# Kernel optimization log

Hardware: AMD Instinct MI355X
Metric: run time of the kernel (lower is better)

The kernel has to match this reference:

```python
import jax, jax.numpy as jnp
import numpy as np

BST_DEPTH = 10                      # tree depth
NB_SPLIT = 2 ** BST_DEPTH - 1       # 1023 internal (split) nodes
NB_NODES = 2 ** (BST_DEPTH + 1) - 1 # 2047 total nodes
N = 32768                           # batch size
IN_SIZE = 255                       # raw feature dim (dim = IN_SIZE + 1 after bias concat)


def setup_inputs() -> dict:
    key = jax.random.key(0)
    k1, k2, k3 = jax.random.split(key, 3)
    dim = IN_SIZE + 1
    X = jax.random.normal(k1, (N, IN_SIZE), dtype=jnp.float32)
    # A ~ U[0,1) as in torch.rand
    A = jax.random.uniform(k2, (NB_SPLIT, dim), dtype=jnp.float32)
    W = jax.random.normal(k3, (1, dim + NB_NODES), dtype=jnp.float32) * 0.02
    b = jnp.zeros((1,), dtype=jnp.float32)
    return {"X": X, "A": A, "W": W, "b": b}


def _latent_tree_z(x, A):
    """Equivalent of LatentTree._compute_q + clamp, unpruned.

    The torch code initializes q=1, scatters min(1, +/-XA) into children, then
    propagates parent mins down for `depth` iterations. The fixed point it
    reaches is exactly q_t = min(q_parent(t), sign_t * XA[:, parent(t)]) computed
    level by level (root q = 1), which is what we build here.
    """
    XA = x @ A.T  # [N, nb_split]
    n = x.shape[0]
    q_levels = [jnp.ones((n, 1), x.dtype)]  # root
    for l in range(1, BST_DEPTH + 1):
        t = np.arange(2 ** l - 1, 2 ** (l + 1) - 1)      # node ids at level l
        parent = (t - 1) // 2                            # split-node ids
        sign = np.where(t % 2 == 1, 1.0, -1.0).astype(np.float32)  # left:+, right:-
        e = XA[:, parent] * sign[None, :]                # edge values [N, 2^l]
        prev_off = 2 ** (l - 1) - 1
        q_parent = q_levels[-1][:, parent - prev_off]    # gather parent q
        q_levels.append(jnp.minimum(q_parent, e))
    q = jnp.concatenate(q_levels, axis=1)  # [N, nb_nodes]
    return jnp.clip(q, 0.0, 1.0)


def reference(X, A, W, b):
    # append bias column of ones
    x = jnp.concatenate([X, jnp.ones((X.shape[0], 1), X.dtype)], axis=1)
    z = _latent_tree_z(x, A)                 # [N, nb_nodes]
    xz = jnp.concatenate([x, z], axis=1)     # [N, dim + nb_nodes]
    return jax.nn.sigmoid(xz @ W.T + b)      # [N, 1]
```

## Files before the change

### kernel.cpp

```cpp
#include <hip/hip_runtime.h>

typedef __attribute__((ext_vector_type(8))) short    bf16x8;
typedef __attribute__((ext_vector_type(4))) float    f32x4;
typedef __attribute__((ext_vector_type(4))) float    float4_t;
typedef __attribute__((ext_vector_type(4))) unsigned u32x4;
typedef __attribute__((ext_vector_type(2))) unsigned u32x2;

constexpr int NSAMP    = 32768;
constexpr int INSZ     = 255;
constexpr int DIM      = 256;
constexpr int NSPLIT   = 1023;
constexpr int NCOL     = 1024;
constexpr int BM       = 32;
constexpr int NTHREADS = 256;
constexpr int NMT      = BM / 16;
constexpr int NPASS    = 64 / 4;

constexpr int XA_OFF    = 16384;
constexpr int PART_OFF  = 8192;
constexpr int PSTRIDE   = 64;
constexpr int LDS_BYTES = XA_OFF + BM * 2048;
constexpr size_t WS_NEED = (size_t)NCOL * DIM * 2;

extern __shared__ char smem[];

__device__ __forceinline__ short f2bf(float f) {
  unsigned x = __builtin_bit_cast(unsigned, f);
  x += 0x7fffu + ((x >> 16) & 1u);
  return (short)(x >> 16);
}
__device__ __forceinline__ float bfraw(unsigned hw16) {
  return __builtin_bit_cast(float, hw16 << 16);
}
__device__ __forceinline__ unsigned cvt_pk(float lo, float hi) {
  unsigned r;
  asm("v_cvt_pk_bf16_f32 %0, %1, %2" : "=v"(r) : "v"(lo), "v"(hi));
  return r;
}
__device__ __forceinline__ float clamp01(float v) {
  return fminf(fmaxf(v, 0.f), 1.f);
}

__global__ void prep_frag(const float* __restrict__ A, const float* __restrict__ W,
                          u32x4* __restrict__ wsf)
{
  int t    = blockIdx.x * 512 + threadIdx.x;
  int lane = t & 63;
  int ks   = (t >> 6) & 7;
  int ct   = t >> 9;
  int col  = ct * 16 + (lane & 15);
  int k0   = ks * 32 + ((lane >> 4) << 3);
  const float* src = (col < NSPLIT) ? (A + col * DIM + k0) : (W + k0);
  float4_t a0 = *(const float4_t*)src;
  float4_t a1 = *(const float4_t*)(src + 4);
  u32x4 p;
  p[0] = cvt_pk(a0[0], a0[1]);
  p[1] = cvt_pk(a0[2], a0[3]);
  p[2] = cvt_pk(a1[0], a1[1]);
  p[3] = cvt_pk(a1[2], a1[3]);
  wsf[t] = p;
}

template<bool USE_WS>
__device__ __forceinline__ void load_bfr(int ct, bf16x8* dst, int lane,
                                         const u32x4* __restrict__ wsf,
                                         const float* __restrict__ A,
                                         const float* __restrict__ W)
{
  if constexpr (USE_WS) {
    const u32x4* fp = wsf + ct * 512 + lane;
#pragma unroll
    for (int ks = 0; ks < 8; ++ks)
      dst[ks] = __builtin_bit_cast(bf16x8, fp[ks * 64]);
  } else {
    int col = ct * 16 + (lane & 15);
    int k0  = (lane >> 4) << 3;
    const float* ap = (col < NSPLIT) ? (A + col * DIM) : W;
#pragma unroll
    for (int ks = 0; ks < 8; ++ks) {
      float4_t a0 = *(const float4_t*)(ap + ks * 32 + k0);
      float4_t a1 = *(const float4_t*)(ap + ks * 32 + k0 + 4);
      u32x4 p;
      p[0] = cvt_pk(a0[0], a0[1]);
      p[1] = cvt_pk(a0[2], a0[3]);
      p[2] = cvt_pk(a1[0], a1[1]);
      p[3] = cvt_pk(a1[2], a1[3]);
      dst[ks] = __builtin_bit_cast(bf16x8, p);
    }
  }
}

__device__ __forceinline__ float walk(const char* __restrict__ xar, int swz, int lane,
                                      const float* __restrict__ wl,
                                      float w7a, float w7b,
                                      const float* __restrict__ w8r,
                                      const float* __restrict__ w9r,
                                      const float* __restrict__ wAr)
{
  float acc = 0.f;
  float q   = 1.0f;
#pragma unroll
  for (int l = 1; l <= 6; ++l) {
    float qp = __shfl(q, lane >> 1, 64);
    int  pos = (1 << (l - 1)) + (lane >> 1);
    unsigned hw = *(const unsigned short*)(xar + (((pos << 1)) ^ swz));
    float xa = bfraw(hw);
    float e  = (lane & 1) ? -xa : xa;
    q = fminf(qp, e);
    acc += clamp01(q) * wl[l - 1];
  }
  unsigned h7 = *(const unsigned short*)(xar + ((((64 + lane) << 1)) ^ swz));
  float xa7 = bfraw(h7);
  float q7a = fminf(q, xa7), q7b = fminf(q, -xa7);
  acc += clamp01(q7a) * w7a + clamp01(q7b) * w7b;
  unsigned u8 = *(const unsigned*)(xar + (((256 + 4 * lane)) ^ swz));
  float x8a = bfraw(u8 & 0xffffu), x8b = bfraw(u8 >> 16);
  float q8[4];
  q8[0] = fminf(q7a, x8a);  q8[1] = fminf(q7a, -x8a);
  q8[2] = fminf(q7b, x8b);  q8[3] = fminf(q7b, -x8b);
#pragma unroll
  for (int c = 0; c < 4; ++c) acc += clamp01(q8[c]) * w8r[c];
  u32x2 u9 = *(const u32x2*)(xar + (((512 + 8 * lane)) ^ swz));
  float x9[4] = { bfraw(u9[0] & 0xffffu), bfraw(u9[0] >> 16),
                  bfraw(u9[1] & 0xffffu), bfraw(u9[1] >> 16) };
  float q9[8];
#pragma unroll
  for (int c = 0; c < 8; ++c)
    q9[c] = fminf(q8[c >> 1], (c & 1) ? -x9[c >> 1] : x9[c >> 1]);
#pragma unroll
  for (int c = 0; c < 8; ++c) acc += clamp01(q9[c]) * w9r[c];
  u32x4 uAB = *(const u32x4*)(xar + (((1024 + 16 * lane)) ^ swz));
  float xA[8] = { bfraw(uAB[0] & 0xffffu), bfraw(uAB[0] >> 16),
                  bfraw(uAB[1] & 0xffffu), bfraw(uAB[1] >> 16),
                  bfraw(uAB[2] & 0xffffu), bfraw(uAB[2] >> 16),
                  bfraw(uAB[3] & 0xffffu), bfraw(uAB[3] >> 16) };
#pragma unroll
  for (int c = 0; c < 16; ++c) {
    float qv = fminf(q9[c >> 1], (c & 1) ? -xA[c >> 1] : xA[c >> 1]);
    acc += clamp01(qv) * wAr[c];
  }
  return acc;
}

template<bool USE_WS>
__global__ __launch_bounds__(NTHREADS) __attribute__((amdgpu_waves_per_eu(2, 2)))
void lt_main(const float* __restrict__ X, const float* __restrict__ A,
             const float* __restrict__ W, const float* __restrict__ Bv,
             const u32x4* __restrict__ wsf, float* __restrict__ Out)
{
  const int tid  = threadIdx.x;
  const int lane = tid & 63;
  const int wave = tid >> 6;
  const int m0   = blockIdx.x * BM;

  bf16x8 b0[8], b1[8];
  load_bfr<USE_WS>(wave, b0, lane, wsf, A, W);

  float wl[6], w8r[4], w9r[8], wAr[16];
#pragma unroll
  for (int l = 1; l <= 6; ++l)
    wl[l - 1] = (lane < (1 << l)) ? W[DIM + (1 << l) - 1 + lane] : 0.f;
  float w7a = W[DIM + 127 + 2 * lane];
  float w7b = W[DIM + 128 + 2 * lane];
#pragma unroll
  for (int e = 0; e < 4; ++e)  w8r[e] = W[DIM + 255 + 4 * lane + e];
#pragma unroll
  for (int e = 0; e < 8; ++e)  w9r[e] = W[DIM + 511 + 8 * lane + e];
#pragma unroll
  for (int e = 0; e < 16; ++e) wAr[e] = W[DIM + 1023 + 16 * lane + e];

  {
    const float4_t* Xt = (const float4_t*)(X + (size_t)m0 * INSZ);
#pragma unroll
    for (int i = 0; i < 8; ++i) {
      int idx = tid + i * NTHREADS;
      if (idx < 2040) {
        float4_t v = Xt[idx];
#pragma unroll
        for (int e = 0; e < 4; ++e) {
          int g   = idx * 4 + e;
          int row = g / 255;
          int col = g - row * 255;
          *(short*)(smem + (((row << 9) + (col << 1)) ^ ((row & 7) << 4))) = f2bf(v[e]);
        }
      }
    }
    if (tid < BM)
      *(short*)(smem + (((tid << 9) + (255 << 1)) ^ ((tid & 7) << 4))) = (short)0x3f80;
  }
  __syncthreads();

  bf16x8 xf[NMT][8];
#pragma unroll
  for (int mt = 0; mt < NMT; ++mt) {
    int row = mt * 16 + (lane & 15);
#pragma unroll
    for (int ks = 0; ks < 8; ++ks) {
      int kk = ks * 32 + ((lane >> 4) << 3);
      xf[mt][ks] = *(const bf16x8*)(smem + (((row << 9) + (kk << 1)) ^ ((row & 7) << 4)));
    }
  }

#pragma unroll
  for (int p = 0; p < NPASS; ++p) {
    bf16x8* cur = (p & 1) ? b1 : b0;
    bf16x8* nxt = (p & 1) ? b0 : b1;
    if (p < NPASS - 1)
      load_bfr<USE_WS>((p + 1) * 4 + wave, nxt, lane, wsf, A, W);

    f32x4 acc[NMT];
#pragma unroll
    for (int mt = 0; mt < NMT; ++mt) acc[mt] = f32x4{0.f, 0.f, 0.f, 0.f};
#pragma unroll
    for (int ks = 0; ks < 8; ++ks) {
#pragma unroll
      for (int mt = 0; mt < NMT; ++mt)
        acc[mt] = __builtin_amdgcn_mfma_f32_16x16x32_bf16(xf[mt][ks], cur[ks], acc[mt], 0, 0, 0);
    }

    int col = (p * 4 + wave) * 16 + (lane & 15);
    int pos = (col < NSPLIT) ? (col + 1) : 0;
#pragma unroll
    for (int mt = 0; mt < NMT; ++mt) {
#pragma unroll
      for (int j = 0; j < 4; ++j) {
        int row = mt * 16 + ((lane >> 4) << 2) + j;
        int byt = XA_OFF + (row << 11) + (((pos << 1)) ^ (((row >> 2) & 3) << 5));
        *(short*)(smem + byt) = f2bf(acc[mt][j]);
      }
    }
  }
  __syncthreads();

  float* part = (float*)(smem + PART_OFF);

#pragma unroll
  for (int t = 0; t < 4; ++t) {
    int rA = wave * 8 + 2 * t;
    int rB = rA + 1;
    const char* xarA = smem + XA_OFF + (rA << 11);
    const char* xarB = smem + XA_OFF + (rB << 11);
    const int swzA = ((rA >> 2) & 3) << 5;
    const int swzB = ((rB >> 2) & 3) << 5;
    float accA = walk(xarA, swzA, lane, wl, w7a, w7b, w8r, w9r, wAr);
    float accB = walk(xarB, swzB, lane, wl, w7a, w7b, w8r, w9r, wAr);
    part[rA * PSTRIDE + lane] = accA;
    part[rB * PSTRIDE + lane] = accB;
  }
  __syncthreads();

  {
    int r = tid >> 3, j = tid & 7;
    const float* pr = part + r * PSTRIDE + j * 8;
    float4_t s0 = *(const float4_t*)pr;
    float4_t s1 = *(const float4_t*)(pr + 4);
    float sum = ((s0[0] + s0[1]) + (s0[2] + s0[3]))
              + ((s1[0] + s1[1]) + (s1[2] + s1[3]));
    sum += __shfl_xor(sum, 1, 64);
    sum += __shfl_xor(sum, 2, 64);
    sum += __shfl_xor(sum, 4, 64);
    if (j == 0) {
      const char* xar = smem + XA_OFF + (r << 11);
      int swz = ((r >> 2) & 3) << 5;
      float xw = bfraw(*(const unsigned short*)(xar + (0 ^ swz)));
      float bias = Bv[0] + W[DIM];
      Out[m0 + r] = 1.f / (1.f + __expf(-(sum + xw + bias)));
    }
  }
}

extern "C" void kernel_launch(void* const* d_in, const int* in_sizes, int n_in,
                              void* d_out, int out_size, void* d_ws, size_t ws_size,
                              hipStream_t stream) {
  (void)in_sizes; (void)n_in; (void)out_size;
  const float* X  = (const float*)d_in[0];
  const float* A  = (const float*)d_in[1];
  const float* W  = (const float*)d_in[2];
  const float* Bv = (const float*)d_in[3];
  float* Out = (float*)d_out;

  const bool use_ws = (d_ws != nullptr) && (ws_size >= WS_NEED);
  if (use_ws) {
    prep_frag<<<64, 512, 0, stream>>>(A, W, (u32x4*)d_ws);
    hipFuncSetAttribute(reinterpret_cast<const void*>(lt_main<true>),
                        hipFuncAttributeMaxDynamicSharedMemorySize, LDS_BYTES);
    lt_main<true><<<NSAMP / BM, NTHREADS, LDS_BYTES, stream>>>(
        X, A, W, Bv, (const u32x4*)d_ws, Out);
  } else {
    hipFuncSetAttribute(reinterpret_cast<const void*>(lt_main<false>),
                        hipFuncAttributeMaxDynamicSharedMemorySize, LDS_BYTES);
    lt_main<false><<<NSAMP / BM, NTHREADS, LDS_BYTES, stream>>>(
        X, A, W, Bv, nullptr, Out);
  }
}
```

Baseline: 44.01 us.

## Transpose XA to node-major layout and walk tree depth-first with wave-wide pruning

Doubles the block to 64 samples and 8 waves, and stores the bf16 XA tile node-major so each lane owns one sample and each tree node is one row. The per-sample level-by-level walk is replaced by a templated depth-first traversal per wave. Each subtree is skipped when a ballot shows no lane has a positive q, since every descendant would clamp to zero. This exact pruning removes most LDS reads and min/clamp/FMA work in deep levels. In exchange it adds branches, more register pressure, and a 160 KB LDS footprint that may limit occupancy.

New measurement: 39.39 us. 1.12x faster.

```diff
diff --git a/kernel.cpp b/kernel.cpp
--- a/kernel.cpp
+++ b/kernel.cpp
@@ -4,22 +4,19 @@
 typedef __attribute__((ext_vector_type(4))) float    f32x4;
 typedef __attribute__((ext_vector_type(4))) float    float4_t;
 typedef __attribute__((ext_vector_type(4))) unsigned u32x4;
-typedef __attribute__((ext_vector_type(2))) unsigned u32x2;
 
 constexpr int NSAMP    = 32768;
 constexpr int INSZ     = 255;
 constexpr int DIM      = 256;
 constexpr int NSPLIT   = 1023;
 constexpr int NCOL     = 1024;
-constexpr int BM       = 32;
-constexpr int NTHREADS = 256;
-constexpr int NMT      = BM / 16;
-constexpr int NPASS    = 64 / 4;
-
-constexpr int XA_OFF    = 16384;
-constexpr int PART_OFF  = 8192;
-constexpr int PSTRIDE   = 64;
-constexpr int LDS_BYTES = XA_OFF + BM * 2048;
+constexpr int BM       = 64;
+constexpr int NTHREADS = 512;
+constexpr int NMT      = 4;
+constexpr int NPASS    = 8;
+
+constexpr int XA_OFF    = 32768;
+constexpr int LDS_BYTES = XA_OFF + NCOL * 128;
 constexpr size_t WS_NEED = (size_t)NCOL * DIM * 2;
 
 extern __shared__ char smem[];
@@ -39,6 +36,14 @@
 }
 __device__ __forceinline__ float clamp01(float v) {
   return fminf(fmaxf(v, 0.f), 1.f);
+}
+
+__device__ __forceinline__ int xat_sw(int node) {
+  return ((node & 15) << 3) | ((node & 1) << 2);
+}
+__device__ __forceinline__ float xat_read(const char* __restrict__ xat, int t, int lane2) {
+  unsigned hw = *(const unsigned short*)(xat + t * 128 + (lane2 ^ xat_sw(t)));
+  return bfraw(hw);
 }
 
 __global__ void prep_frag(const float* __restrict__ A, const float* __restrict__ W,
@@ -80,66 +85,30 @@
     for (int ks = 0; ks < 8; ++ks) {
       float4_t a0 = *(const float4_t*)(ap + ks * 32 + k0);
       float4_t a1 = *(const float4_t*)(ap + ks * 32 + k0 + 4);
-      u32x4 p;
-      p[0] = cvt_pk(a0[0], a0[1]);
-      p[1] = cvt_pk(a0[2], a0[3]);
-      p[2] = cvt_pk(a1[0], a1[1]);
-      p[3] = cvt_pk(a1[2], a1[3]);
+      unsigned q0 = ((unsigned)(unsigned short)f2bf(a0[0])) | (((unsigned)(unsigned short)f2bf(a0[1])) << 16);
+      unsigned q1 = ((unsigned)(unsigned short)f2bf(a0[2])) | (((unsigned)(unsigned short)f2bf(a0[3])) << 16);
+      unsigned q2 = ((unsigned)(unsigned short)f2bf(a1[0])) | (((unsigned)(unsigned short)f2bf(a1[1])) << 16);
+      unsigned q3 = ((unsigned)(unsigned short)f2bf(a1[2])) | (((unsigned)(unsigned short)f2bf(a1[3])) << 16);
+      u32x4 p = {q0, q1, q2, q3};
       dst[ks] = __builtin_bit_cast(bf16x8, p);
     }
   }
 }
 
-__device__ __forceinline__ float walk(const char* __restrict__ xar, int swz, int lane,
-                                      const float* __restrict__ wl,
-                                      float w7a, float w7b,
-                                      const float* __restrict__ w8r,
-                                      const float* __restrict__ w9r,
-                                      const float* __restrict__ wAr)
-{
-  float acc = 0.f;
-  float q   = 1.0f;
-#pragma unroll
-  for (int l = 1; l <= 6; ++l) {
-    float qp = __shfl(q, lane >> 1, 64);
-    int  pos = (1 << (l - 1)) + (lane >> 1);
-    unsigned hw = *(const unsigned short*)(xar + (((pos << 1)) ^ swz));
-    float xa = bfraw(hw);
-    float e  = (lane & 1) ? -xa : xa;
-    q = fminf(qp, e);
-    acc += clamp01(q) * wl[l - 1];
-  }
-  unsigned h7 = *(const unsigned short*)(xar + ((((64 + lane) << 1)) ^ swz));
-  float xa7 = bfraw(h7);
-  float q7a = fminf(q, xa7), q7b = fminf(q, -xa7);
-  acc += clamp01(q7a) * w7a + clamp01(q7b) * w7b;
-  unsigned u8 = *(const unsigned*)(xar + (((256 + 4 * lane)) ^ swz));
-  float x8a = bfraw(u8 & 0xffffu), x8b = bfraw(u8 >> 16);
-  float q8[4];
-  q8[0] = fminf(q7a, x8a);  q8[1] = fminf(q7a, -x8a);
-  q8[2] = fminf(q7b, x8b);  q8[3] = fminf(q7b, -x8b);
-#pragma unroll
-  for (int c = 0; c < 4; ++c) acc += clamp01(q8[c]) * w8r[c];
-  u32x2 u9 = *(const u32x2*)(xar + (((512 + 8 * lane)) ^ swz));
-  float x9[4] = { bfraw(u9[0] & 0xffffu), bfraw(u9[0] >> 16),
-                  bfraw(u9[1] & 0xffffu), bfraw(u9[1] >> 16) };
-  float q9[8];
-#pragma unroll
-  for (int c = 0; c < 8; ++c)
-    q9[c] = fminf(q8[c >> 1], (c & 1) ? -x9[c >> 1] : x9[c >> 1]);
-#pragma unroll
-  for (int c = 0; c < 8; ++c) acc += clamp01(q9[c]) * w9r[c];
-  u32x4 uAB = *(const u32x4*)(xar + (((1024 + 16 * lane)) ^ swz));
-  float xA[8] = { bfraw(uAB[0] & 0xffffu), bfraw(uAB[0] >> 16),
-                  bfraw(uAB[1] & 0xffffu), bfraw(uAB[1] >> 16),
-                  bfraw(uAB[2] & 0xffffu), bfraw(uAB[2] >> 16),
-                  bfraw(uAB[3] & 0xffffu), bfraw(uAB[3] >> 16) };
-#pragma unroll
-  for (int c = 0; c < 16; ++c) {
-    float qv = fminf(q9[c >> 1], (c & 1) ? -xA[c >> 1] : xA[c >> 1]);
-    acc += clamp01(qv) * wAr[c];
-  }
-  return acc;
+template<int D>
+__device__ __forceinline__ void dfs(int t, float q, float& acc,
+                                    const char* __restrict__ xat, int lane2,
+                                    const float* __restrict__ Wz)
+{
+  if (__ballot(q > 0.f) == 0ull) return;
+  float xa = xat_read(xat, t, lane2);
+  float qL = fminf(q, xa);
+  float qR = fminf(q, -xa);
+  acc += clamp01(qL) * Wz[2 * t + 1] + clamp01(qR) * Wz[2 * t + 2];
+  if constexpr (D > 1) {
+    dfs<D - 1>(2 * t + 1, qL, acc, xat, lane2, Wz);
+    dfs<D - 1>(2 * t + 2, qR, acc, xat, lane2, Wz);
+  }
 }
 
 template<bool USE_WS>
@@ -156,25 +125,12 @@
   bf16x8 b0[8], b1[8];
   load_bfr<USE_WS>(wave, b0, lane, wsf, A, W);
 
-  float wl[6], w8r[4], w9r[8], wAr[16];
-#pragma unroll
-  for (int l = 1; l <= 6; ++l)
-    wl[l - 1] = (lane < (1 << l)) ? W[DIM + (1 << l) - 1 + lane] : 0.f;
-  float w7a = W[DIM + 127 + 2 * lane];
-  float w7b = W[DIM + 128 + 2 * lane];
-#pragma unroll
-  for (int e = 0; e < 4; ++e)  w8r[e] = W[DIM + 255 + 4 * lane + e];
-#pragma unroll
-  for (int e = 0; e < 8; ++e)  w9r[e] = W[DIM + 511 + 8 * lane + e];
-#pragma unroll
-  for (int e = 0; e < 16; ++e) wAr[e] = W[DIM + 1023 + 16 * lane + e];
-
   {
     const float4_t* Xt = (const float4_t*)(X + (size_t)m0 * INSZ);
 #pragma unroll
     for (int i = 0; i < 8; ++i) {
       int idx = tid + i * NTHREADS;
-      if (idx < 2040) {
+      if (idx < 4080) {
         float4_t v = Xt[idx];
 #pragma unroll
         for (int e = 0; e < 4; ++e) {
@@ -201,12 +157,14 @@
     }
   }
 
+  char* xat = smem + XA_OFF;
+
 #pragma unroll
   for (int p = 0; p < NPASS; ++p) {
     bf16x8* cur = (p & 1) ? b1 : b0;
     bf16x8* nxt = (p & 1) ? b0 : b1;
     if (p < NPASS - 1)
-      load_bfr<USE_WS>((p + 1) * 4 + wave, nxt, lane, wsf, A, W);
+      load_bfr<USE_WS>((p + 1) * 8 + wave, nxt, lane, wsf, A, W);
 
     f32x4 acc[NMT];
 #pragma unroll
@@ -218,54 +176,50 @@
         acc[mt] = __builtin_amdgcn_mfma_f32_16x16x32_bf16(xf[mt][ks], cur[ks], acc[mt], 0, 0, 0);
     }
 
-    int col = (p * 4 + wave) * 16 + (lane & 15);
-    int pos = (col < NSPLIT) ? (col + 1) : 0;
+    int node = (p * 8 + wave) * 16 + (lane & 15);
+    int sw   = xat_sw(node);
+    char* xrow = xat + node * 128;
 #pragma unroll
     for (int mt = 0; mt < NMT; ++mt) {
 #pragma unroll
-      for (int j = 0; j < 4; ++j) {
-        int row = mt * 16 + ((lane >> 4) << 2) + j;
-        int byt = XA_OFF + (row << 11) + (((pos << 1)) ^ (((row >> 2) & 3) << 5));
-        *(short*)(smem + byt) = f2bf(acc[mt][j]);
+      for (int h = 0; h < 2; ++h) {
+        int s0 = mt * 16 + ((lane >> 4) << 2) + h * 2;
+        unsigned lo = (unsigned short)f2bf(acc[mt][2 * h]);
+        unsigned hi = (unsigned short)f2bf(acc[mt][2 * h + 1]);
+        *(unsigned*)(xrow + ((s0 * 2) ^ sw)) = lo | (hi << 16);
       }
     }
   }
   __syncthreads();
 
-  float* part = (float*)(smem + PART_OFF);
-
-#pragma unroll
-  for (int t = 0; t < 4; ++t) {
-    int rA = wave * 8 + 2 * t;
-    int rB = rA + 1;
-    const char* xarA = smem + XA_OFF + (rA << 11);
-    const char* xarB = smem + XA_OFF + (rB << 11);
-    const int swzA = ((rA >> 2) & 3) << 5;
-    const int swzB = ((rB >> 2) & 3) << 5;
-    float accA = walk(xarA, swzA, lane, wl, w7a, w7b, w8r, w9r, wAr);
-    float accB = walk(xarB, swzB, lane, wl, w7a, w7b, w8r, w9r, wAr);
-    part[rA * PSTRIDE + lane] = accA;
-    part[rB * PSTRIDE + lane] = accB;
-  }
+  const float* Wz    = W + DIM;
+  const int    lane2 = lane << 1;
+
+  int s3 = 7 + wave;
+  int a2 = (s3 - 1) >> 1;
+  int a1 = (a2 - 1) >> 1;
+  float q = 1.f;
+  {
+    float x0 = xat_read(xat, 0,  lane2); q = fminf(q, (a1 & 1) ? x0 : -x0);
+    float x1 = xat_read(xat, a1, lane2); q = fminf(q, (a2 & 1) ? x1 : -x1);
+    float x2 = xat_read(xat, a2, lane2); q = fminf(q, (s3 & 1) ? x2 : -x2);
+  }
+  float acc = 0.f;
+  dfs<7>(s3, q, acc, xat, lane2, Wz);
+  if (wave == 0)
+    dfs<3>(0, 1.f, acc, xat, lane2, Wz);
+
+  float* part = (float*)smem;
+  part[(wave << 6) + lane] = acc;
   __syncthreads();
 
-  {
-    int r = tid >> 3, j = tid & 7;
-    const float* pr = part + r * PSTRIDE + j * 8;
-    float4_t s0 = *(const float4_t*)pr;
-    float4_t s1 = *(const float4_t*)(pr + 4);
-    float sum = ((s0[0] + s0[1]) + (s0[2] + s0[3]))
-              + ((s1[0] + s1[1]) + (s1[2] + s1[3]));
-    sum += __shfl_xor(sum, 1, 64);
-    sum += __shfl_xor(sum, 2, 64);
-    sum += __shfl_xor(sum, 4, 64);
-    if (j == 0) {
-      const char* xar = smem + XA_OFF + (r << 11);
-      int swz = ((r >> 2) & 3) << 5;
-      float xw = bfraw(*(const unsigned short*)(xar + (0 ^ swz)));
-      float bias = Bv[0] + W[DIM];
-      Out[m0 + r] = 1.f / (1.f + __expf(-(sum + xw + bias)));
-    }
+  if (tid < BM) {
+    float sum = 0.f;
+#pragma unroll
+    for (int w = 0; w < 8; ++w) sum += part[(w << 6) + tid];
+    float xw = xat_read(xat, 1023, tid << 1);
+    float v  = sum + xw + Bv[0] + Wz[0];
+    Out[m0 + tid] = 1.f / (1.f + __expf(-v));
   }
 }
 
```
